# Kernel tuning notes

Hardware: AMD Instinct MI355X
Metric: run time of the kernel (lower is better)

The kernel has to match this reference:

```python
import jax, jax.numpy as jnp
import numpy as np

D_MODEL = 1024
N_HEADS = 16
HEAD_DIM = D_MODEL // N_HEADS
ROPE_BASE = 10000.0


def rotate_half(x):
    x1, x2 = x[..., : x.shape[-1] // 2], x[..., x.shape[-1] // 2 :]
    return jnp.concatenate((-x2, x1), axis=-1)


def rope_cos_sin(L, dim, dtype):
    inv_freq = 1.0 / (ROPE_BASE ** (jnp.arange(0, dim, 2, dtype=jnp.float32) / dim))
    freqs = jnp.arange(L, dtype=jnp.float32)[:, None] * inv_freq[None, :]  # [L, dim/2]
    emb = jnp.concatenate((freqs, freqs), axis=-1)  # [L, dim]
    # broadcast over batch and heads: [1, L, 1, dim]
    return jnp.cos(emb)[None, :, None, :].astype(dtype), jnp.sin(emb)[None, :, None, :].astype(dtype)


def setup_inputs() -> dict:
    key = jax.random.key(0)
    ks = jax.random.split(key, 11)
    N, L, S = 2, 2048, 2048
    s = 1.0 / np.sqrt(D_MODEL)
    return {
        "queries": jax.random.normal(ks[0], (N, L, D_MODEL), jnp.float32),
        "keys": jax.random.normal(ks[1], (N, S, D_MODEL), jnp.float32),
        "values": jax.random.normal(ks[2], (N, S, D_MODEL), jnp.float32),
        "Wq": jax.random.normal(ks[3], (D_MODEL, D_MODEL), jnp.float32) * s,
        "bq": jnp.zeros((D_MODEL,), jnp.float32),
        "Wk": jax.random.normal(ks[4], (D_MODEL, D_MODEL), jnp.float32) * s,
        "bk": jnp.zeros((D_MODEL,), jnp.float32),
        "Wv": jax.random.normal(ks[5], (D_MODEL, D_MODEL), jnp.float32) * s,
        "bv": jnp.zeros((D_MODEL,), jnp.float32),
        "Wo": jax.random.normal(ks[6], (D_MODEL, D_MODEL), jnp.float32) * s,
        "bo": jnp.zeros((D_MODEL,), jnp.float32),
    }


def reference(queries, keys, values, Wq, bq, Wk, bk, Wv, bv, Wo, bo):
    N, L, _ = queries.shape
    S = keys.shape[1]
    H, hd = N_HEADS, HEAD_DIM

    # QKV projections (nn.Linear: x @ W.T + b), reshape to [N, T, H, hd]
    q = (jnp.einsum("nld,ed->nle", queries, Wq) + bq).reshape(N, L, H, hd)
    k = (jnp.einsum("nsd,ed->nse", keys, Wk) + bk).reshape(N, S, H, hd)
    v = (jnp.einsum("nsd,ed->nse", values, Wv) + bv).reshape(N, S, H, hd)

    # Rotary embedding: q*cos + rotate_half(q)*sin  (same for k)
    cos, sin = rope_cos_sin(L, hd, q.dtype)
    q = q * cos + rotate_half(q) * sin
    k = k * cos + rotate_half(k) * sin

    # Inner attention: scaled dot-product with causal mask
    scores = jnp.einsum("nlhd,nshd->nhls", q, k) / jnp.sqrt(jnp.asarray(hd, q.dtype))
    causal = jnp.tril(jnp.ones((L, S), bool))
    scores = jnp.where(causal[None, None], scores, jnp.asarray(-1e9, scores.dtype))
    attn = jax.nn.softmax(scores, axis=-1)
    out = jnp.einsum("nhls,nshd->nlhd", attn, v).reshape(N, L, H * hd)

    # Output projection
    return jnp.einsum("nle,de->nld", out, Wo) + bo
```

## Files before the change

kernel.cpp:

```cpp
#include <hip/hip_runtime.h>
#include <math.h>

#define DM 1024
#define NH 16
#define HD 64
#define SEQ 2048
#define NB2 2
#define MROWS 4096

typedef unsigned short u16;
typedef __attribute__((ext_vector_type(8))) short short8;
typedef __attribute__((ext_vector_type(4))) float f32x4;
typedef __attribute__((ext_vector_type(2))) unsigned int u32x2;

#define GLOAD16(g, l) __builtin_amdgcn_global_load_lds( \
    (const __attribute__((address_space(1))) void*)(g),  \
    (__attribute__((address_space(3))) void*)(l), 16, 0, 0)

static __device__ __forceinline__ u16 f2bf(float f) {
  union { float f; unsigned u; } v; v.f = f;
  unsigned r = v.u + 0x7fffu + ((v.u >> 16) & 1u);
  return (u16)(r >> 16);
}

static __device__ __forceinline__ short8 cvt8(float4 a, float4 b) {
  short8 s;
  s[0] = (short)f2bf(a.x); s[1] = (short)f2bf(a.y);
  s[2] = (short)f2bf(a.z); s[3] = (short)f2bf(a.w);
  s[4] = (short)f2bf(b.x); s[5] = (short)f2bf(b.y);
  s[6] = (short)f2bf(b.z); s[7] = (short)f2bf(b.w);
  return s;
}

__global__ void conv_all(
    const float* __restrict__ q, const float* __restrict__ k, const float* __restrict__ v,
    const float* __restrict__ wq, const float* __restrict__ wk,
    const float* __restrict__ wv, const float* __restrict__ wo,
    u16* __restrict__ xq, u16* __restrict__ xk, u16* __restrict__ xv,
    u16* __restrict__ wqb, u16* __restrict__ wkb, u16* __restrict__ wvb, u16* __restrict__ wob,
    float* __restrict__ cosT, float* __restrict__ sinT)
{
  const int z = blockIdx.z;
  const int idx = blockIdx.x * blockDim.x + threadIdx.x;
  if (z == 7) {
    if (idx >= SEQ * 32) return;
    int l = idx >> 5, i = idx & 31;
    float invf = expf(-(float)i * (9.210340371976184f / 32.0f));
    float ang = (float)l * invf;
    float s, c;
    sincosf(ang, &s, &c);
    cosT[idx] = c; sinT[idx] = s;
    return;
  }
  const float* src; u16* dst; int n;
  switch (z) {
    case 0: src = q;  dst = xq;  n = MROWS * DM; break;
    case 1: src = k;  dst = xk;  n = MROWS * DM; break;
    case 2: src = v;  dst = xv;  n = MROWS * DM; break;
    case 3: src = wq; dst = wqb; n = DM * DM; break;
    case 4: src = wk; dst = wkb; n = DM * DM; break;
    case 5: src = wv; dst = wvb; n = DM * DM; break;
    default: src = wo; dst = wob; n = DM * DM; break;
  }
  const int base = idx * 8;
  if (base >= n) return;
  float4 a = *(const float4*)(src + base);
  float4 b = *(const float4*)(src + base + 4);
  *(short8*)(dst + base) = cvt8(a, b);
}

#define VSTR 136
template<int EPI>
__device__ __forceinline__ void gemm_body(
    u16* SH,
    const u16* __restrict__ A, const u16* __restrict__ W,
    const float* __restrict__ bias,
    u16* __restrict__ Cb, float* __restrict__ Cf, u16* __restrict__ VT,
    const float* __restrict__ cosT, const float* __restrict__ sinT,
    float qscale, int row0, int col0)
{
  const int tid = threadIdx.x;
  const int lane = tid & 63;
  const int wid = tid >> 6;
  const int wr = wid & 3;
  const int wc = wid >> 2;
  const int fr = lane & 15, kg = lane >> 4;

  const u16* ga = A + (size_t)(row0 + (tid & 127)) * DM + ((tid >> 7) << 3);
  const u16* gb = W + (size_t)(col0 + (tid & 127)) * DM + ((tid >> 7) << 3);
  const int ldsw = wid * 512;
  const int aoffL = kg * 1024 + (wr * 32 + fr) * 8;
  const int boffL = 4096 + kg * 1024 + (wc * 64 + fr) * 8;

  u16* B0 = SH;
  u16* B1 = SH + 8192;
  u16* B2 = SH + 16384;

  f32x4 acc[2][4];
#pragma unroll
  for (int m = 0; m < 2; ++m)
#pragma unroll
    for (int n = 0; n < 4; ++n) acc[m][n] = (f32x4){0.f, 0.f, 0.f, 0.f};

  auto issue = [&](int t, u16* buf) {
    const int ko = t * 32;
    GLOAD16(ga + ko, buf + ldsw);
    GLOAD16(gb + ko, buf + 4096 + ldsw);
  };
  auto compute = [&](const u16* buf) {
    short8 afr[2], bfr[4];
#pragma unroll
    for (int m = 0; m < 2; ++m)
      afr[m] = *(const short8*)(&buf[aoffL + m * 128]);
#pragma unroll
    for (int n = 0; n < 4; ++n)
      bfr[n] = *(const short8*)(&buf[boffL + n * 128]);
#pragma unroll
    for (int m = 0; m < 2; ++m)
#pragma unroll
      for (int n = 0; n < 4; ++n)
        acc[m][n] = __builtin_amdgcn_mfma_f32_16x16x32_bf16(afr[m], bfr[n], acc[m][n], 0, 0, 0);
  };

  issue(0, B0);
  issue(1, B1);

#define STEP2(t, bufR, bufW) do {                                   \
    asm volatile("s_waitcnt vmcnt(2)" ::: "memory");                \
    __builtin_amdgcn_sched_barrier(0);                              \
    __builtin_amdgcn_s_barrier();                                   \
    __builtin_amdgcn_sched_barrier(0);                              \
    if ((t) + 2 < 32) issue((t) + 2, bufW);                         \
    compute(bufR);                                                  \
  } while (0)
#define STEP0(t, bufR) do {                                         \
    asm volatile("s_waitcnt vmcnt(0)" ::: "memory");                \
    __builtin_amdgcn_sched_barrier(0);                              \
    __builtin_amdgcn_s_barrier();                                   \
    __builtin_amdgcn_sched_barrier(0);                              \
    compute(bufR);                                                  \
  } while (0)

  for (int t = 0; t < 30; t += 3) {
    STEP2(t,     B0, B2);
    STEP2(t + 1, B1, B0);
    STEP2(t + 2, B2, B1);
  }
  STEP2(30, B0, B2);
  STEP0(31, B1);
#undef STEP2
#undef STEP0

  if (EPI == 2) {
    __syncthreads();
    const int nb = row0 >> 11;
    const int sbase = row0 & (SEQ - 1);
#pragma unroll
    for (int p = 0; p < 2; ++p) {
      if (wc == p) {
#pragma unroll
        for (int n = 0; n < 4; ++n) {
          const int dcol = n * 16 + fr;
          const float bv = bias[col0 + p * 64 + dcol];
#pragma unroll
          for (int m = 0; m < 2; ++m)
#pragma unroll
            for (int r = 0; r < 4; ++r)
              SH[dcol * VSTR + wr * 32 + m * 16 + kg * 4 + r] = f2bf(acc[m][n][r] + bv);
        }
      }
      __syncthreads();
      {
        const int dcol = tid >> 3, sq = tid & 7;
        const int e = col0 + p * 64 + dcol;
        u16* dst = VT + ((size_t)(nb * NH + (e >> 6)) * HD + (e & 63)) * SEQ + sbase + sq * 16;
        *(short8*)(dst)     = *(const short8*)(&SH[dcol * VSTR + sq * 16]);
        *(short8*)(dst + 8) = *(const short8*)(&SH[dcol * VSTR + sq * 16 + 8]);
      }
      __syncthreads();
    }
    return;
  }

#pragma unroll
  for (int m = 0; m < 2; ++m) {
#pragma unroll
    for (int r = 0; r < 4; ++r) {
      const int rowg = row0 + wr * 32 + m * 16 + kg * 4 + r;
      if (EPI == 1) {
#pragma unroll
        for (int n = 0; n < 4; ++n) {
          const int colg = col0 + wc * 64 + n * 16 + fr;
          Cf[(size_t)rowg * DM + colg] = acc[m][n][r] + bias[colg];
        }
      } else {
        const int l = rowg & (SEQ - 1);
#pragma unroll
        for (int n = 0; n < 4; ++n) {
          const int colg = col0 + wc * 64 + n * 16 + fr;
          const int i = n * 16 + fr;
          const int fi = i & 31;
          const float c = cosT[l * 32 + fi];
          const float s = sinT[l * 32 + fi];
          const float v = acc[m][n][r] + bias[colg];
          const float pv = acc[m][n ^ 2][r] + bias[col0 + wc * 64 + ((n ^ 2) * 16 + fr)];
          const float o = v * c + ((i < 32) ? -pv : pv) * s;
          Cb[(size_t)rowg * DM + colg] = f2bf(o * qscale);
        }
      }
    }
  }
}

__global__ __launch_bounds__(512) void gemm_qkv(
    const u16* __restrict__ Xq, const u16* __restrict__ Xk, const u16* __restrict__ Xv,
    const u16* __restrict__ Wqb, const u16* __restrict__ Wkb, const u16* __restrict__ Wvb,
    const float* __restrict__ bq, const float* __restrict__ bk, const float* __restrict__ bv,
    u16* __restrict__ Qb, u16* __restrict__ Kb, u16* __restrict__ VT,
    const float* __restrict__ cosT, const float* __restrict__ sinT)
{
  __shared__ __align__(16) u16 SH[24576];
  const int z = blockIdx.z;
  const int row0 = blockIdx.x * 128, col0 = blockIdx.y * 128;
  if (z == 2) {
    gemm_body<2>(SH, Xv, Wvb, bv, nullptr, nullptr, VT, nullptr, nullptr, 1.0f, row0, col0);
  } else if (z == 0) {
    gemm_body<0>(SH, Xq, Wqb, bq, Qb, nullptr, nullptr, cosT, sinT, 0.125f, row0, col0);
  } else {
    gemm_body<0>(SH, Xk, Wkb, bk, Kb, nullptr, nullptr, cosT, sinT, 1.0f, row0, col0);
  }
}

__global__ __launch_bounds__(512) void gemm_o(
    const u16* __restrict__ Ob, const u16* __restrict__ Wob,
    const float* __restrict__ bo, float* __restrict__ out)
{
  __shared__ __align__(16) u16 SH[24576];
  gemm_body<1>(SH, Ob, Wob, bo, nullptr, out, nullptr, nullptr, nullptr, 1.0f,
               blockIdx.x * 128, blockIdx.y * 128);
}

__global__ __launch_bounds__(512) void flash_attn(
    const u16* __restrict__ Qp, const u16* __restrict__ Kp,
    const u16* __restrict__ VT, u16* __restrict__ Op)
{
  __shared__ __align__(16) u16 Ks[4096];
  __shared__ __align__(16) u16 Vt[4096];
  __shared__ __align__(16) u16 Pl[9216];

  const int tid = threadIdx.x;
  const int lane = tid & 63;
  const int w = tid >> 6;
  const int fr = lane & 15, rg = lane >> 4;
  const int qbp = blockIdx.x;
  const int h = blockIdx.y, nb = blockIdx.z;

  const size_t headoff = (size_t)nb * SEQ * DM + (size_t)h * HD;
  const size_t vthead = (size_t)(nb * NH + h) * HD * SEQ;
  const int srow = tid >> 3;
  const int sch  = tid & 7;
  u16* Pw = &Pl[w * 1152];

  for (int pass = 0; pass < 2; ++pass) {
    const int qe = pass ? (15 - qbp) : qbp;
    const int KBend = 2 * qe + 2;
    const int qrow0 = qe * 128 + w * 16;
    const int qg = qrow0 + fr;

    short8 qf[2];
#pragma unroll
    for (int ck = 0; ck < 2; ++ck)
      qf[ck] = *(const short8*)(Qp + headoff + (size_t)(qrow0 + fr) * DM + ck * 32 + rg * 8);

    f32x4 accO[4];
#pragma unroll
    for (int df = 0; df < 4; ++df) accO[df] = (f32x4){0.f, 0.f, 0.f, 0.f};
    float m_run = -3e38f, l_run = 0.f;

    short8 kpf = *(const short8*)(Kp + headoff + (size_t)srow * DM + sch * 8);
    short8 vpf = *(const short8*)(VT + vthead + (size_t)srow * SEQ + sch * 8);

    for (int kb = 0; kb < KBend; ++kb) {
      *(short8*)(&Ks[(sch * 64 + (srow ^ sch)) * 8]) = kpf;
      *(short8*)(&Vt[(sch * 64 + (srow ^ sch)) * 8]) = vpf;
      __syncthreads();
      if (kb + 1 < KBend) {
        kpf = *(const short8*)(Kp + headoff + (size_t)((kb + 1) * 64 + srow) * DM + sch * 8);
        vpf = *(const short8*)(VT + vthead + (size_t)srow * SEQ + (kb + 1) * 64 + sch * 8);
      }

      const bool active = (kb * 64) <= (qrow0 + 15);
      if (active) {
        short8 kf[4][2];
#pragma unroll
        for (int sf = 0; sf < 4; ++sf)
#pragma unroll
          for (int ck = 0; ck < 2; ++ck) {
            const int dc = ck * 4 + rg;
            kf[sf][ck] = *(const short8*)(&Ks[(dc * 64 + ((sf * 16 + fr) ^ dc)) * 8]);
          }
        f32x4 sc_[4];
#pragma unroll
        for (int sf = 0; sf < 4; ++sf) {
          f32x4 z = (f32x4){0.f, 0.f, 0.f, 0.f};
#pragma unroll
          for (int ck = 0; ck < 2; ++ck)
            z = __builtin_amdgcn_mfma_f32_16x16x32_bf16(kf[sf][ck], qf[ck], z, 0, 0, 0);
          sc_[sf] = z;
        }
        float rowmax = -3e38f;
#pragma unroll
        for (int sf = 0; sf < 4; ++sf)
#pragma unroll
          for (int r = 0; r < 4; ++r) {
            const int sg = kb * 64 + sf * 16 + rg * 4 + r;
            float v = sc_[sf][r];
            v = (sg <= qg) ? v : -3e38f;
            sc_[sf][r] = v;
            rowmax = fmaxf(rowmax, v);
          }
        rowmax = fmaxf(rowmax, __shfl_xor(rowmax, 16, 64));
        rowmax = fmaxf(rowmax, __shfl_xor(rowmax, 32, 64));
        const float mnew = fmaxf(m_run, rowmax);
        const float scl = __expf(m_run - mnew);
        m_run = mnew;
        float psum = 0.f;
#pragma unroll
        for (int sf = 0; sf < 4; ++sf)
#pragma unroll
          for (int r = 0; r < 4; ++r) {
            const float p = __expf(sc_[sf][r] - mnew);
            sc_[sf][r] = p;
            psum += p;
          }
        psum += __shfl_xor(psum, 16, 64);
        psum += __shfl_xor(psum, 32, 64);
        l_run = l_run * scl + psum;
        const float s0 = __shfl(scl, rg * 4 + 0, 64);
        const float s1 = __shfl(scl, rg * 4 + 1, 64);
        const float s2 = __shfl(scl, rg * 4 + 2, 64);
        const float s3 = __shfl(scl, rg * 4 + 3, 64);
#pragma unroll
        for (int df = 0; df < 4; ++df) {
          accO[df][0] *= s0; accO[df][1] *= s1;
          accO[df][2] *= s2; accO[df][3] *= s3;
        }
#pragma unroll
        for (int sf = 0; sf < 4; ++sf) {
          u32x2 pv;
          pv[0] = (unsigned)f2bf(sc_[sf][0]) | ((unsigned)f2bf(sc_[sf][1]) << 16);
          pv[1] = (unsigned)f2bf(sc_[sf][2]) | ((unsigned)f2bf(sc_[sf][3]) << 16);
          *(u32x2*)(&Pw[fr * 72 + (sf * 8 + rg * 2) * 2]) = pv;
        }
        short8 pa[2];
#pragma unroll
        for (int ck = 0; ck < 2; ++ck)
          pa[ck] = *(const short8*)(&Pw[fr * 72 + (ck * 16 + rg * 4) * 2]);
#pragma unroll
        for (int df = 0; df < 4; ++df)
#pragma unroll
          for (int ck = 0; ck < 2; ++ck) {
            const int sc = ck * 4 + rg;
            const short8 vf = *(const short8*)(&Vt[(sc * 64 + ((df * 16 + fr) ^ sc)) * 8]);
            accO[df] = __builtin_amdgcn_mfma_f32_16x16x32_bf16(pa[ck], vf, accO[df], 0, 0, 0);
          }
      }
      __syncthreads();
    }

    const float l0 = __shfl(l_run, rg * 4 + 0, 64);
    const float l1 = __shfl(l_run, rg * 4 + 1, 64);
    const float l2 = __shfl(l_run, rg * 4 + 2, 64);
    const float l3 = __shfl(l_run, rg * 4 + 3, 64);
#pragma unroll
    for (int df = 0; df < 4; ++df) {
      const int d = df * 16 + fr;
      Op[headoff + (size_t)(qrow0 + rg * 4 + 0) * DM + d] = f2bf(accO[df][0] / l0);
      Op[headoff + (size_t)(qrow0 + rg * 4 + 1) * DM + d] = f2bf(accO[df][1] / l1);
      Op[headoff + (size_t)(qrow0 + rg * 4 + 2) * DM + d] = f2bf(accO[df][2] / l2);
      Op[headoff + (size_t)(qrow0 + rg * 4 + 3) * DM + d] = f2bf(accO[df][3] / l3);
    }
  }
}

extern "C" void kernel_launch(void* const* d_in, const int* in_sizes, int n_in,
                              void* d_out, int out_size, void* d_ws, size_t ws_size,
                              hipStream_t stream) {
  (void)in_sizes; (void)n_in; (void)out_size; (void)ws_size;
  const float* queries = (const float*)d_in[0];
  const float* keys    = (const float*)d_in[1];
  const float* values  = (const float*)d_in[2];
  const float* Wq = (const float*)d_in[3];
  const float* bq = (const float*)d_in[4];
  const float* Wk = (const float*)d_in[5];
  const float* bk = (const float*)d_in[6];
  const float* Wv = (const float*)d_in[7];
  const float* bv = (const float*)d_in[8];
  const float* Wo = (const float*)d_in[9];
  const float* bo = (const float*)d_in[10];
  float* out = (float*)d_out;

  char* ws = (char*)d_ws;
  const size_t MB = 1u << 20;
  u16* Qb  = (u16*)(ws);
  u16* Kb  = (u16*)(ws + 8 * MB);
  u16* VTg = (u16*)(ws + 16 * MB);
  u16* Xq  = (u16*)(ws + 24 * MB);
  u16* Ob  = Xq;
  u16* Xk  = (u16*)(ws + 32 * MB);
  u16* Xv  = (u16*)(ws + 40 * MB);
  u16* Wqb = (u16*)(ws + 48 * MB);
  u16* Wkb = (u16*)(ws + 50 * MB);
  u16* Wvb = (u16*)(ws + 52 * MB);
  u16* Wob = (u16*)(ws + 54 * MB);
  float* cosT = (float*)(ws + 56 * MB);
  float* sinT = (float*)(ws + 56 * MB + 256 * 1024);

  conv_all<<<dim3(2048, 1, 8), 256, 0, stream>>>(
      queries, keys, values, Wq, Wk, Wv, Wo,
      Xq, Xk, Xv, Wqb, Wkb, Wvb, Wob, cosT, sinT);
  gemm_qkv<<<dim3(MROWS / 128, DM / 128, 3), 512, 0, stream>>>(
      Xq, Xk, Xv, Wqb, Wkb, Wvb, bq, bk, bv, Qb, Kb, VTg, cosT, sinT);
  flash_attn<<<dim3(SEQ / 256, NH, NB2), 512, 0, stream>>>(Qb, Kb, VTg, Ob);
  gemm_o<<<dim3(MROWS / 128, DM / 128), 512, 0, stream>>>(Ob, Wob, bo, out);
}
```

Before: 148.2 us.

## Switch GEMM mainloop to double-buffered 64-wide K tiles with MFMA priority

The projection GEMM mainloop moves from a triple-buffered pipeline with 32-wide K steps and explicit vmcnt waits to a double-buffered pipeline with 64-wide K steps. This halves the number of barriers per tile. Each step issues four direct-to-LDS loads and runs two MFMA sub-steps, and s_setprio raises wave priority around the MFMA block. LDS per block grows from 48KB to 64KB, which may reduce occupancy. The loop now depends on __syncthreads to make the previous prefetch visible, so it loses the partial-wait overlap of the old scheme.

Result: no change. 149.4 us (+0.8%).

```diff
diff --git a/kernel.cpp b/kernel.cpp
--- a/kernel.cpp
+++ b/kernel.cpp
@@ -88,13 +88,9 @@
 
   const u16* ga = A + (size_t)(row0 + (tid & 127)) * DM + ((tid >> 7) << 3);
   const u16* gb = W + (size_t)(col0 + (tid & 127)) * DM + ((tid >> 7) << 3);
-  const int ldsw = wid * 512;
-  const int aoffL = kg * 1024 + (wr * 32 + fr) * 8;
-  const int boffL = 4096 + kg * 1024 + (wc * 64 + fr) * 8;
-
+  const int lw = wid * 512;
   u16* B0 = SH;
-  u16* B1 = SH + 8192;
-  u16* B2 = SH + 16384;
+  u16* B1 = SH + 16384;
 
   f32x4 acc[2][4];
 #pragma unroll
@@ -103,53 +99,40 @@
     for (int n = 0; n < 4; ++n) acc[m][n] = (f32x4){0.f, 0.f, 0.f, 0.f};
 
   auto issue = [&](int t, u16* buf) {
-    const int ko = t * 32;
-    GLOAD16(ga + ko, buf + ldsw);
-    GLOAD16(gb + ko, buf + 4096 + ldsw);
+    const int ko = t * 64;
+    GLOAD16(ga + ko, buf + lw);
+    GLOAD16(ga + ko + 32, buf + lw + 4096);
+    GLOAD16(gb + ko, buf + 8192 + lw);
+    GLOAD16(gb + ko + 32, buf + 8192 + lw + 4096);
   };
-  auto compute = [&](const u16* buf) {
+  auto compute = [&](const u16* buf, int kk) {
+    const int kc = kk * 4 + kg;
     short8 afr[2], bfr[4];
 #pragma unroll
     for (int m = 0; m < 2; ++m)
-      afr[m] = *(const short8*)(&buf[aoffL + m * 128]);
+      afr[m] = *(const short8*)(&buf[kc * 1024 + (wr * 32 + m * 16 + fr) * 8]);
 #pragma unroll
     for (int n = 0; n < 4; ++n)
-      bfr[n] = *(const short8*)(&buf[boffL + n * 128]);
+      bfr[n] = *(const short8*)(&buf[8192 + kc * 1024 + (wc * 64 + n * 16 + fr) * 8]);
+    __builtin_amdgcn_s_setprio(1);
 #pragma unroll
     for (int m = 0; m < 2; ++m)
 #pragma unroll
       for (int n = 0; n < 4; ++n)
         acc[m][n] = __builtin_amdgcn_mfma_f32_16x16x32_bf16(afr[m], bfr[n], acc[m][n], 0, 0, 0);
+    __builtin_amdgcn_s_setprio(0);
   };
 
   issue(0, B0);
-  issue(1, B1);
-
-#define STEP2(t, bufR, bufW) do {                                   \
-    asm volatile("s_waitcnt vmcnt(2)" ::: "memory");                \
-    __builtin_amdgcn_sched_barrier(0);                              \
-    __builtin_amdgcn_s_barrier();                                   \
-    __builtin_amdgcn_sched_barrier(0);                              \
-    if ((t) + 2 < 32) issue((t) + 2, bufW);                         \
-    compute(bufR);                                                  \
-  } while (0)
-#define STEP0(t, bufR) do {                                         \
-    asm volatile("s_waitcnt vmcnt(0)" ::: "memory");                \
-    __builtin_amdgcn_sched_barrier(0);                              \
-    __builtin_amdgcn_s_barrier();                                   \
-    __builtin_amdgcn_sched_barrier(0);                              \
-    compute(bufR);                                                  \
-  } while (0)
-
-  for (int t = 0; t < 30; t += 3) {
-    STEP2(t,     B0, B2);
-    STEP2(t + 1, B1, B0);
-    STEP2(t + 2, B2, B1);
-  }
-  STEP2(30, B0, B2);
-  STEP0(31, B1);
-#undef STEP2
-#undef STEP0
+  const int KT = DM / 64;
+  for (int t = 0; t < KT; ++t) {
+    u16* bufR = (t & 1) ? B1 : B0;
+    u16* bufW = (t & 1) ? B0 : B1;
+    __syncthreads();
+    if (t + 1 < KT) issue(t + 1, bufW);
+    compute(bufR, 0);
+    compute(bufR, 1);
+  }
 
   if (EPI == 2) {
     __syncthreads();
@@ -219,7 +202,7 @@
     u16* __restrict__ Qb, u16* __restrict__ Kb, u16* __restrict__ VT,
     const float* __restrict__ cosT, const float* __restrict__ sinT)
 {
-  __shared__ __align__(16) u16 SH[24576];
+  __shared__ __align__(16) u16 SH[32768];
   const int z = blockIdx.z;
   const int row0 = blockIdx.x * 128, col0 = blockIdx.y * 128;
   if (z == 2) {
@@ -235,7 +218,7 @@
     const u16* __restrict__ Ob, const u16* __restrict__ Wob,
     const float* __restrict__ bo, float* __restrict__ out)
 {
-  __shared__ __align__(16) u16 SH[24576];
+  __shared__ __align__(16) u16 SH[32768];
   gemm_body<1>(SH, Ob, Wob, bo, nullptr, out, nullptr, nullptr, nullptr, 1.0f,
                blockIdx.x * 128, blockIdx.y * 128);
 }
```
